# Kernel tuning notes

Measured on AMD Instinct MI355X. Metric: run time of the kernel, lower is better.

The kernel has to match this reference:

```python
import jax, jax.numpy as jnp
import numpy as np

NUM_HEADS = 8
WINDOW = 3
LOCAL_LEN = WINDOW * WINDOW
SR_RATIO = 8


def _normalize(v, eps=1e-12):
    n = jnp.linalg.norm(v, axis=-1, keepdims=True)
    return v / jnp.maximum(n, eps)


def _layernorm(v, g, b, eps=1e-5):
    m = v.mean(-1, keepdims=True)
    var = ((v - m) ** 2).mean(-1, keepdims=True)
    return (v - m) / jnp.sqrt(var + eps) * g + b


def _unfold3(x, H, W):
    # x: [B, C, H, W] -> [B, C, 9, H*W]  (kernel 3, pad 1, stride 1; torch nn.Unfold layout)
    B, C = x.shape[0], x.shape[1]
    xp = jnp.pad(x, ((0, 0), (0, 0), (1, 1), (1, 1)))
    patches = jnp.stack([xp[:, :, di:di + H, dj:dj + W]
                         for di in range(WINDOW) for dj in range(WINDOW)], axis=2)
    return patches.reshape(B, C, LOCAL_LEN, H * W)


def _forward(x, relative_coords_table, seq_length_scale, q_w, q_b, kv_w, kv_b,
             temperature, query_embedding, sr_w, sr_b, norm_g, norm_b,
             cpb_fc1_w, cpb_fc1_b, cpb_fc2_w, cpb_fc2_b,
             rel_bias_local, learnable_tokens, learnable_bias,
             proj_w, proj_b, relative_pos_index, padding_mask, H, W):
    B, N, C = x.shape
    hd = C // NUM_HEADS
    pool_H, pool_W = H // SR_RATIO, W // SR_RATIO
    pool_len = pool_H * pool_W

    # ---- queries ----
    q = (x @ q_w.T + q_b).reshape(B, N, NUM_HEADS, hd).transpose(0, 2, 1, 3)  # [B,h,N,d]
    q_norm = _normalize(q)
    q_scaled = (q_norm + query_embedding) * jax.nn.softplus(temperature) * seq_length_scale

    # ---- local k/v via unfold ----
    kv = x @ kv_w.T + kv_b  # [B,N,2C]
    k_loc = _normalize(kv[..., :C].reshape(B, N, NUM_HEADS, hd)).reshape(B, N, C)
    kv_img = jnp.concatenate([k_loc, kv[..., C:]], -1).transpose(0, 2, 1).reshape(B, 2 * C, H, W)
    kv_unf = _unfold3(kv_img, H, W).reshape(B, 2 * NUM_HEADS, hd, LOCAL_LEN, N)
    kv_unf = kv_unf.transpose(0, 1, 4, 2, 3)  # [B,2h,N,d,9]
    k_local, v_local = kv_unf[:, :NUM_HEADS], kv_unf[:, NUM_HEADS:]

    attn_local = jnp.einsum('bhnd,bhndl->bhnl', q_scaled, k_local) + rel_bias_local[:, None, :]
    attn_local = jnp.where(padding_mask, -jnp.inf, attn_local)

    # ---- pooled global k/v ----
    x_img = x.transpose(0, 2, 1).reshape(B, C, H, W)
    x_sr = jax.nn.gelu(jnp.einsum('oc,bchw->bohw', sr_w, x_img) + sr_b[None, :, None, None],
                       approximate=False)
    x_pool = x_sr.reshape(B, C, pool_H, SR_RATIO, pool_W, SR_RATIO).mean((3, 5))
    x_pool = x_pool.reshape(B, C, pool_len).transpose(0, 2, 1)
    x_pool = _layernorm(x_pool, norm_g, norm_b)
    kv_p = (x_pool @ kv_w.T + kv_b).reshape(B, pool_len, 2 * NUM_HEADS, hd).transpose(0, 2, 1, 3)
    k_pool, v_pool = kv_p[:, :NUM_HEADS], kv_p[:, NUM_HEADS:]

    # ---- continuous relative position bias (extrapolation path) ----
    cpb = jax.nn.relu(relative_coords_table @ cpb_fc1_w.T + cpb_fc1_b) @ cpb_fc2_w.T + cpb_fc2_b  # [T,h]
    pool_bias = cpb[relative_pos_index].reshape(N, pool_len, NUM_HEADS).transpose(2, 0, 1)  # [h,N,P]

    attn_pool = jnp.einsum('bhnd,bhpd->bhnp', q_scaled, _normalize(k_pool)) + pool_bias

    attn = jax.nn.softmax(jnp.concatenate([attn_local, attn_pool], -1), axis=-1)
    a_loc, a_pool = attn[..., :LOCAL_LEN], attn[..., LOCAL_LEN:]

    lt = jnp.einsum('bhnd,hdl->bhnl', q_norm, learnable_tokens) + learnable_bias + a_loc
    x_local = jnp.einsum('bhnl,bhndl->bhnd', lt, v_local)
    x_p = jnp.einsum('bhnp,bhpd->bhnd', a_pool, v_pool)
    out = (x_local + x_p).transpose(0, 2, 1, 3).reshape(B, N, C)
    return out @ proj_w.T + proj_b


def setup_inputs() -> dict:
    key = jax.random.key(0)
    B, H, W, C = 4, 64, 64, 256
    N = H * W
    hd = C // NUM_HEADS
    pool_H, pool_W = H // SR_RATIO, W // SR_RATIO
    pool_len = pool_H * pool_W

    # padding mask + per-query valid window length (get_seqlen_and_mask)
    ii, jj = np.meshgrid(np.arange(H), np.arange(W), indexing='ij')
    cols = []
    for di in range(WINDOW):
        for dj in range(WINDOW):
            ni, nj = ii + di - 1, jj + dj - 1
            cols.append(((ni < 0) | (ni >= H) | (nj < 0) | (nj >= W)).reshape(-1))
    padding_mask = np.stack(cols, -1)  # [N, 9], True = outside image
    local_len = (~padding_mask).sum(-1, keepdims=True).astype(np.float32)
    seq_length_scale = np.log(local_len + pool_len)  # [N, 1]

    # get_relative_position_cpb((H,W), (pool_H,pool_W))
    axis_q = np.arange(H, dtype=np.float64)
    axis_k = axis_q.reshape(pool_H, SR_RATIO).mean(-1)
    kh, kw = np.meshgrid(axis_k, axis_k, indexing='ij')
    qh, qw = np.meshgrid(axis_q, axis_q, indexing='ij')
    rel_h = (qh.ravel()[:, None] - kh.ravel()[None, :]) / (H - 1) * 8
    rel_w = (qw.ravel()[:, None] - kw.ravel()[None, :]) / (W - 1) * 8
    rel = np.stack([rel_h, rel_w], -1).reshape(-1, 2)
    table, idx = np.unique(rel, axis=0, return_inverse=True)
    table = np.sign(table) * np.log2(np.abs(table) + 1.0) / np.log2(8.0)

    ks = jax.random.split(key, 12)

    def nrm(k, shape, std=0.02):
        return jax.random.normal(k, shape, jnp.float32) * std

    return {
        'x': jax.random.normal(ks[0], (B, N, C), jnp.float32),
        'relative_coords_table': jnp.asarray(table, jnp.float32),
        'seq_length_scale': jnp.asarray(seq_length_scale, jnp.float32),
        'q_w': nrm(ks[1], (C, C)), 'q_b': jnp.zeros((C,), jnp.float32),
        'kv_w': nrm(ks[2], (2 * C, C)), 'kv_b': jnp.zeros((2 * C,), jnp.float32),
        'temperature': jnp.full((NUM_HEADS, 1, 1), float(np.log(np.expm1(1.0 / 0.24))), jnp.float32),
        'query_embedding': nrm(ks[3], (NUM_HEADS, 1, hd)),
        'sr_w': nrm(ks[4], (C, C)), 'sr_b': jnp.zeros((C,), jnp.float32),
        'norm_g': jnp.ones((C,), jnp.float32), 'norm_b': jnp.zeros((C,), jnp.float32),
        'cpb_fc1_w': nrm(ks[5], (512, 2), 0.1), 'cpb_fc1_b': jnp.zeros((512,), jnp.float32),
        'cpb_fc2_w': nrm(ks[6], (NUM_HEADS, 512)), 'cpb_fc2_b': jnp.zeros((NUM_HEADS,), jnp.float32),
        'rel_bias_local': nrm(ks[7], (NUM_HEADS, LOCAL_LEN), 0.0004),
        'learnable_tokens': nrm(ks[8], (NUM_HEADS, hd, LOCAL_LEN)),
        'learnable_bias': jnp.zeros((NUM_HEADS, 1, LOCAL_LEN), jnp.float32),
        'proj_w': nrm(ks[9], (C, C)), 'proj_b': jnp.zeros((C,), jnp.float32),
        'relative_pos_index': jnp.asarray(idx, jnp.int32),
        'padding_mask': jnp.asarray(padding_mask),
        'H': H, 'W': W,
    }


def reference(x, relative_coords_table, seq_length_scale, q_w, q_b, kv_w, kv_b,
              temperature, query_embedding, sr_w, sr_b, norm_g, norm_b,
              cpb_fc1_w, cpb_fc1_b, cpb_fc2_w, cpb_fc2_b,
              rel_bias_local, learnable_tokens, learnable_bias,
              proj_w, proj_b, relative_pos_index, padding_mask, H, W):
    return _forward(x, relative_coords_table, seq_length_scale, q_w, q_b, kv_w, kv_b,
                    temperature, query_embedding, sr_w, sr_b, norm_g, norm_b,
                    cpb_fc1_w, cpb_fc1_b, cpb_fc2_w, cpb_fc2_b,
                    rel_bias_local, learnable_tokens, learnable_bias,
                    proj_w, proj_b, relative_pos_index, padding_mask, H, W)
```

## Files before the change

### kernel.cpp

```cpp
#include <hip/hip_runtime.h>
#include <math.h>


typedef unsigned short ushort_t;
typedef __attribute__((ext_vector_type(8))) _Float16 half8;
typedef __attribute__((ext_vector_type(2))) _Float16 half2_t;
typedef __attribute__((ext_vector_type(4))) float f32x4;

static __device__ __forceinline__ ushort_t f2h(float f) {
    _Float16 h = (_Float16)f;
    return *(ushort_t*)&h;
}

static __device__ __forceinline__ float fdot2f(half2_t a, half2_t b, float c) {
#if __has_builtin(__builtin_amdgcn_fdot2)
    return __builtin_amdgcn_fdot2(a, b, c, false);
#else
    return (float)a[0] * (float)b[0] + (float)a[1] * (float)b[1] + c;
#endif
}

template <int CTRL>
static __device__ __forceinline__ float dpp_addf(float x) {
    int v = __builtin_amdgcn_update_dpp(
        0, __builtin_bit_cast(int, x), CTRL, 0xF, 0xF, true);
    return x + __builtin_bit_cast(float, v);
}
static __device__ __forceinline__ float quad_sumf(float x) {
    return dpp_addf<0x4E>(dpp_addf<0xB1>(x));
}
static __device__ __forceinline__ float sum16f(float x) {
    return dpp_addf<0x128>(dpp_addf<0x124>(quad_sumf(x)));
}

#define GLOAD16(g, l)                                                        \
    __builtin_amdgcn_global_load_lds(                                        \
        (const __attribute__((address_space(1))) unsigned int*)(g),          \
        (__attribute__((address_space(3))) unsigned int*)(l), 16, 0, 0)

template <int TM, int TN, bool AHM>
__global__ __launch_bounds__(256) void mfma_hgemm(
    const ushort_t* __restrict__ Ag, const ushort_t* __restrict__ Bg,
    const float* __restrict__ bias, float* __restrict__ out0,
    ushort_t* __restrict__ qh_out, ushort_t* __restrict__ kvh,
    ushort_t* __restrict__ xsrh, int mode, int Arows)
{
    const int K = 256;
    const int IM = TM / 32;
    const int JN = TN / 32;
    constexpr int LPS = TM / 64 + TN / 64;
    __shared__ ushort_t Ah[2][TM * 32];
    __shared__ ushort_t Bh[2][TN * 32];

    const int t = threadIdx.x;
    const int w = t >> 6;
    const int lane = t & 63;

    const int nwg = gridDim.x * gridDim.y;
    int wg = blockIdx.y * gridDim.x + blockIdx.x;
    wg = (wg & 7) * (nwg >> 3) + (wg >> 3);
    const int bm = (wg / gridDim.x) * TM;
    const int bn = (wg % gridDim.x) * TN;

    const int wm = (w >> 1) * (TM / 2);
    const int wn = (w & 1) * (TN / 2);

    f32x4 acc[IM][JN];
#pragma unroll
    for (int i = 0; i < IM; ++i)
#pragma unroll
        for (int j = 0; j < JN; ++j) acc[i][j] = f32x4{0.f, 0.f, 0.f, 0.f};

    const int lrow  = t >> 2;
    const int lk8sw = ((t & 3) ^ ((t >> 3) & 3)) * 8;

#define STAGE(bufi, k0s)                                                     \
    do {                                                                     \
        _Pragma("unroll")                                                    \
        for (int r = 0; r < TM / 64; ++r) {                                  \
            const ushort_t* srcA = AHM                                       \
                ? Ag + ((size_t)((k0s) >> 5) * Arows + (bm + r * 64 + lrow)) * 32 + lk8sw \
                : Ag + (size_t)(bm + r * 64 + lrow) * K + (k0s) + lk8sw;     \
            GLOAD16(srcA, &Ah[bufi][(unsigned)(r * 64 + w * 16) * 32]);      \
        }                                                                    \
        _Pragma("unroll")                                                    \
        for (int r = 0; r < TN / 64; ++r)                                    \
            GLOAD16(Bg + (size_t)(bn + r * 64 + lrow) * K + (k0s) + lk8sw,   \
                    &Bh[bufi][(unsigned)(r * 64 + w * 16) * 32]);            \
    } while (0)

    const int fr   = lane & 15;
    const int sws8 = ((lane >> 4) ^ ((fr >> 1) & 3)) * 8;

#define COMPUTE(bufi)                                                        \
    do {                                                                     \
        half8 af[IM], bf[JN];                                                \
        _Pragma("unroll")                                                    \
        for (int i2 = 0; i2 < IM; ++i2)                                      \
            af[i2] = *(const half8*)&Ah[bufi][(unsigned)(wm + i2 * 16 + fr) * 32 + sws8]; \
        _Pragma("unroll")                                                    \
        for (int j2 = 0; j2 < JN; ++j2)                                      \
            bf[j2] = *(const half8*)&Bh[bufi][(unsigned)(wn + j2 * 16 + fr) * 32 + sws8]; \
        __builtin_amdgcn_s_setprio(1);                                       \
        _Pragma("unroll")                                                    \
        for (int i2 = 0; i2 < IM; ++i2)                                      \
            _Pragma("unroll")                                                \
            for (int j2 = 0; j2 < JN; ++j2)                                  \
                acc[i2][j2] = __builtin_amdgcn_mfma_f32_16x16x32_f16(        \
                    af[i2], bf[j2], acc[i2][j2], 0, 0, 0);                   \
        __builtin_amdgcn_s_setprio(0);                                       \
    } while (0)

    STAGE(0, 0);
    STAGE(1, 32);
    int buf = 0;
#pragma unroll
    for (int s = 0; s < K / 32 - 1; ++s) {
        asm volatile("s_waitcnt vmcnt(%0)" :: "n"(LPS) : "memory");
        __builtin_amdgcn_s_barrier();
        asm volatile("" ::: "memory");
        COMPUTE(buf);
        asm volatile("" ::: "memory");
        __builtin_amdgcn_s_barrier();
        asm volatile("" ::: "memory");
        if (s + 2 < K / 32) STAGE(buf, (s + 2) * 32);
        buf ^= 1;
    }
    asm volatile("s_waitcnt vmcnt(0)" ::: "memory");
    __builtin_amdgcn_s_barrier();
    asm volatile("" ::: "memory");
    COMPUTE(buf);
#undef COMPUTE
#undef STAGE

    const int q4 = (lane >> 4) * 4;
#pragma unroll
    for (int i = 0; i < IM; ++i) {
#pragma unroll
        for (int jp = 0; jp < JN / 2; ++jp) {
#pragma unroll
            for (int r = 0; r < 4; ++r) {
                const int row = bm + wm + i * 16 + q4 + r;
                const int col0 = bn + wn + jp * 32 + fr;
                const int col1 = col0 + 16;
                float v0 = acc[i][2 * jp][r] + bias[col0];
                float v1 = acc[i][2 * jp + 1][r] + bias[col1];
                if (mode == 0) {
                    if (col0 < 256) {
                        const size_t base = ((size_t)(col0 >> 5) * Arows + row) * 32;
                        qh_out[base + fr]      = f2h(v0);
                        qh_out[base + fr + 16] = f2h(v1);
                    } else if (col0 < 512) {
                        const float ss = sum16f(v0 * v0 + v1 * v1);
                        const float invn = 1.0f / fmaxf(sqrtf(ss), 1e-12f);
                        const size_t base = ((size_t)((col0 - 256) >> 5) * Arows + row) * 64;
                        kvh[base + fr]      = f2h(v0 * invn);
                        kvh[base + fr + 16] = f2h(v1 * invn);
                    } else if (col0 < 768) {
                        const size_t base = ((size_t)((col0 - 512) >> 5) * Arows + row) * 64 + 32;
                        kvh[base + fr]      = f2h(v0);
                        kvh[base + fr + 16] = f2h(v1);
                    } else {
                        v0 = 0.5f * v0 * (1.0f + erff(v0 * 0.70710678118654752f));
                        v1 = 0.5f * v1 * (1.0f + erff(v1 * 0.70710678118654752f));
                        xsrh[(size_t)row * 256 + (col0 - 768)] = f2h(v0);
                        xsrh[(size_t)row * 256 + (col1 - 768)] = f2h(v1);
                    }
                } else if (mode == 2) {
                    if (col0 < 256) {
                        const float ss = sum16f(v0 * v0 + v1 * v1);
                        const float invn = 1.0f / fmaxf(sqrtf(ss), 1e-12f);
                        const size_t base = ((size_t)(col0 >> 5) * Arows + row) * 64;
                        kvh[base + fr]      = f2h(v0 * invn);
                        kvh[base + fr + 16] = f2h(v1 * invn);
                    } else {
                        const size_t base = ((size_t)((col0 - 256) >> 5) * Arows + row) * 64 + 32;
                        kvh[base + fr]      = f2h(v0);
                        kvh[base + fr + 16] = f2h(v1);
                    }
                } else {
                    out0[(size_t)row * 256 + col0] = v0;
                    out0[(size_t)row * 256 + col1] = v1;
                }
            }
        }
    }
}

__global__ __launch_bounds__(256) void prep_cpb(
    const float4* __restrict__ x, ushort4* __restrict__ xh, int n4, int nprep,
    const float* __restrict__ qw, const float* __restrict__ kvw,
    const float* __restrict__ srw, const float* __restrict__ pw,
    const float* __restrict__ qb, const float* __restrict__ kvb,
    const float* __restrict__ srb,
    ushort_t* __restrict__ Wall, ushort_t* __restrict__ Pw,
    float* __restrict__ ball,
    const float* __restrict__ table, const float* __restrict__ w1,
    const float* __restrict__ b1, const float* __restrict__ w2,
    const float* __restrict__ b2, float* __restrict__ outc, int T)
{
    if (blockIdx.x >= nprep) {
        const int wv = threadIdx.x >> 6;
        const int lane = threadIdx.x & 63;
        const int row = (blockIdx.x - nprep) * 4 + wv;
        if (row >= T) return;
        const float t0 = table[(size_t)row * 2];
        const float t1 = table[(size_t)row * 2 + 1];
        const int base = lane * 8;

        const float4* w1p = (const float4*)(w1 + (size_t)base * 2);
        float4 wa = w1p[0], wb = w1p[1], wc = w1p[2], wd = w1p[3];
        float4 ba = *(const float4*)(b1 + base);
        float4 bb = *(const float4*)(b1 + base + 4);
        float h[8];
        h[0] = fmaxf(fmaf(t1, wa.y, fmaf(t0, wa.x, ba.x)), 0.f);
        h[1] = fmaxf(fmaf(t1, wa.w, fmaf(t0, wa.z, ba.y)), 0.f);
        h[2] = fmaxf(fmaf(t1, wb.y, fmaf(t0, wb.x, ba.z)), 0.f);
        h[3] = fmaxf(fmaf(t1, wb.w, fmaf(t0, wb.z, ba.w)), 0.f);
        h[4] = fmaxf(fmaf(t1, wc.y, fmaf(t0, wc.x, bb.x)), 0.f);
        h[5] = fmaxf(fmaf(t1, wc.w, fmaf(t0, wc.z, bb.y)), 0.f);
        h[6] = fmaxf(fmaf(t1, wd.y, fmaf(t0, wd.x, bb.z)), 0.f);
        h[7] = fmaxf(fmaf(t1, wd.w, fmaf(t0, wd.z, bb.w)), 0.f);

#pragma unroll
        for (int hh = 0; hh < 8; ++hh) {
            const float4* w2p = (const float4*)(w2 + (size_t)hh * 512 + base);
            float4 p0 = w2p[0], p1 = w2p[1];
            float s = h[0]*p0.x + h[1]*p0.y + h[2]*p0.z + h[3]*p0.w
                    + h[4]*p1.x + h[5]*p1.y + h[6]*p1.z + h[7]*p1.w;
#pragma unroll
            for (int off = 1; off <= 32; off <<= 1) s += __shfl_xor(s, off);
            if (lane == 0) outc[(size_t)row * 8 + hh] = s + b2[hh];
        }
        return;
    }

    int idx = blockIdx.x * 256 + threadIdx.x;
    if (idx < n4) {
        float4 v = x[idx];
        ushort4 h;
        h.x = f2h(v.x); h.y = f2h(v.y); h.z = f2h(v.z); h.w = f2h(v.w);
        xh[idx] = h;
    }
    if (idx < 262144) {
        int nn = idx >> 8, k = idx & 255;
        float a;
        if (nn < 256)      a = qw[nn * 256 + k];
        else if (nn < 768) a = kvw[(nn - 256) * 256 + k];
        else               a = srw[(nn - 768) * 256 + k];
        Wall[idx] = f2h(a);
    }
    if (idx < 65536) Pw[idx] = f2h(pw[idx]);
    if (idx < 1024) {
        float bv;
        if (idx < 256)      bv = qb[idx];
        else if (idx < 768) bv = kvb[idx - 256];
        else                bv = srb[idx - 768];
        ball[idx] = bv;
    }
}

__global__ __launch_bounds__(256) void pool_ln(
    const ushort_t* __restrict__ xsr, const float* __restrict__ g,
    const float* __restrict__ be, ushort_t* __restrict__ xpool, int Hh, int Ww)
{
    const int C = 256;
    const int Nn = Hh * Ww;
    int b = blockIdx.x >> 6;
    int pidx = blockIdx.x & 63;
    int ph = pidx >> 3, pw = pidx & 7;
    int tid = threadIdx.x;
    float s = 0.f;
    for (int si = 0; si < 8; ++si) {
        int i = ph * 8 + si;
        const ushort_t* rowp = xsr + ((size_t)b * Nn + (size_t)i * Ww + pw * 8) * C + tid;
#pragma unroll
        for (int sj = 0; sj < 8; ++sj)
            s += (float)(*(const _Float16*)&rowp[(size_t)sj * C]);
    }
    s *= (1.f / 64.f);
    __shared__ float red[256];
    red[tid] = s; __syncthreads();
    for (int st = 128; st; st >>= 1) { if (tid < st) red[tid] += red[tid + st]; __syncthreads(); }
    float mean = red[0] * (1.f / 256.f);
    __syncthreads();
    float dv = s - mean;
    red[tid] = dv * dv; __syncthreads();
    for (int st = 128; st; st >>= 1) { if (tid < st) red[tid] += red[tid + st]; __syncthreads(); }
    float var = red[0] * (1.f / 256.f);
    xpool[(size_t)blockIdx.x * C + tid] = f2h(dv * rsqrtf(var + 1e-5f) * g[tid] + be[tid]);
}

__global__ __launch_bounds__(256) void attn_v9(
    const ushort_t* __restrict__ qh_g,
    const ushort_t* __restrict__ kvh,
    const ushort_t* __restrict__ kvph,
    const int* __restrict__ rpi,
    const float* __restrict__ cpbB,
    const float* __restrict__ sls, const float* __restrict__ temp,
    const float* __restrict__ qe, const float* __restrict__ rbl,
    const float* __restrict__ ltok, const float* __restrict__ lbias,
    ushort_t* __restrict__ attno,
    int Mtot)
{
    const int h = blockIdx.y, b = blockIdx.z;
    const int t = threadIdx.x;
    const int i = blockIdx.x;
    const int w = t >> 6;
    const int lane = t & 63;

    __shared__ ushort_t kvloc[3 * 64 * 64];
    __shared__ ushort_t kvp[64 * 64];
    __shared__ ushort_t pb_s[64][66];
    __shared__ float lts[9][32];
    __shared__ float rbl_s[9], lb_s[9], qe_s[32];

    {
        const int lt8 = lane >> 3, ls = lane & 7;
#pragma unroll
        for (int it = 0; it < 6; ++it) {
            const int u = it * 4 + w;
            const int dr = u >> 3, kB = u & 7;
            const int srcRow = min(max(i - 1 + dr, 0), 63);
            const int tok = kB * 8 + lt8;
            GLOAD16(kvh + ((size_t)h * Mtot + b * 4096 + srcRow * 64) * 64
                        + (size_t)(tok * 8 + (ls ^ (tok & 7))) * 8,
                    &kvloc[(size_t)(dr * 64 + kB * 8) * 64]);
        }
#pragma unroll
        for (int it = 0; it < 2; ++it) {
            const int u = it * 4 + w;
            const int tok = u * 8 + lt8;
            GLOAD16(kvph + ((size_t)h * 256 + b * 64) * 64
                         + (size_t)(tok * 8 + (ls ^ (tok & 7))) * 8,
                    &kvp[(size_t)(u * 8) * 64]);
        }
    }
    {
        const int rbase = i * 4096;
        for (int u = t; u < 4096; u += 256) {
            const int idx = rpi[rbase + u];
            pb_s[u >> 6][u & 63] = f2h(cpbB[(size_t)idx * 8 + h]);
        }
        for (int u = t; u < 288; u += 256) lts[u % 9][u / 9] = ltok[h * 288 + u];
        if (t < 9)  { rbl_s[t] = rbl[h * 9 + t]; lb_s[t] = lbias[h * 9 + t]; }
        if (t >= 64 && t < 96) qe_s[t - 64] = qe[h * 32 + (t - 64)];
    }
    __syncthreads();

    const int qi = lane >> 2;
    const int g4 = lane & 3;
    const int co = g4 * 8;
    const int j = w * 16 + qi;
    const int n = i * 64 + j;
    const size_t gq = (size_t)b * 4096 + n;

    const float tm = temp[h];
    const float sp = (tm > 20.f) ? tm : log1pf(expf(tm));

    float qv[8];
    {
        const half8 q8 = *(const half8*)(qh_g + ((size_t)h * Mtot + gq) * 32 + co);
        float ss = 0.f;
#pragma unroll
        for (int d = 0; d < 8; ++d) { qv[d] = (float)q8[d]; ss += qv[d] * qv[d]; }
        ss = quad_sumf(ss);
        const float invn = 1.0f / fmaxf(sqrtf(ss), 1e-12f);
#pragma unroll
        for (int d = 0; d < 8; ++d) qv[d] *= invn;
    }

    float lt[9];
#pragma unroll
    for (int l = 0; l < 9; ++l) {
        float dl = 0.f;
        const float4* lw = (const float4*)&lts[l][co];
#pragma unroll
        for (int c4 = 0; c4 < 2; ++c4) {
            float4 w4 = lw[c4];
            dl += qv[4*c4+0]*w4.x + qv[4*c4+1]*w4.y + qv[4*c4+2]*w4.z + qv[4*c4+3]*w4.w;
        }
        dl = quad_sumf(dl);
        lt[l] = dl + lb_s[l];
    }

    const float scal = sp * sls[n];
    half2_t qh[4];
#pragma unroll
    for (int c = 0; c < 4; ++c) {
        float a = (qv[2*c+0] + qe_s[co + 2*c+0]) * scal;
        float bq = (qv[2*c+1] + qe_s[co + 2*c+1]) * scal;
        qh[c] = half2_t{(_Float16)a, (_Float16)bq};
    }

    float sl[9];
#pragma unroll
    for (int l = 0; l < 9; ++l) {
        const int di = l / 3 - 1, dj = l % 3 - 1;
        const int ii = i + di;
        const int jn = j + dj;
        const bool ok = (ii >= 0) && (ii < 64) && (jn >= 0) && (jn < 64);
        const int dr = di + 1;
        const int tokc = max(min(jn, 63), 0);
        const half8 k8 = *(const half8*)
            &kvloc[(size_t)((dr * 64 + tokc) * 8 + (g4 ^ (tokc & 7))) * 8];
        float dk = 0.f;
        dk = fdot2f(qh[0], __builtin_shufflevector(k8, k8, 0, 1), dk);
        dk = fdot2f(qh[1], __builtin_shufflevector(k8, k8, 2, 3), dk);
        dk = fdot2f(qh[2], __builtin_shufflevector(k8, k8, 4, 5), dk);
        dk = fdot2f(qh[3], __builtin_shufflevector(k8, k8, 6, 7), dk);
        dk = quad_sumf(dk);
        sl[l] = ok ? (dk + rbl_s[l]) : -INFINITY;
    }

    float m = sl[0];
#pragma unroll
    for (int l = 1; l < 9; ++l) m = fmaxf(m, sl[l]);

    half2_t oh[4];
#pragma unroll
    for (int c = 0; c < 4; ++c) oh[c] = half2_t{(_Float16)0.f, (_Float16)0.f};
    float Z = 0.f;

    for (int cch = 0; cch < 8; ++cch) {
        float s8[8];
        float pbv[8];
#pragma unroll
        for (int c = 0; c < 4; ++c) {
            const half2_t p2 = *(const half2_t*)&pb_s[j][cch * 8 + 2 * c];
            pbv[2*c]   = (float)p2[0];
            pbv[2*c+1] = (float)p2[1];
        }
#pragma unroll
        for (int k = 0; k < 8; ++k) {
            const int p = cch * 8 + k;
            const half8 k8 = *(const half8*)
                &kvp[(size_t)(p * 8 + (g4 ^ (p & 7))) * 8];
            float acc = 0.f;
            acc = fdot2f(qh[0], __builtin_shufflevector(k8, k8, 0, 1), acc);
            acc = fdot2f(qh[1], __builtin_shufflevector(k8, k8, 2, 3), acc);
            acc = fdot2f(qh[2], __builtin_shufflevector(k8, k8, 4, 5), acc);
            acc = fdot2f(qh[3], __builtin_shufflevector(k8, k8, 6, 7), acc);
            acc = quad_sumf(acc);
            s8[k] = acc + pbv[k];
        }
        float cmax = s8[0];
#pragma unroll
        for (int k = 1; k < 8; ++k) cmax = fmaxf(cmax, s8[k]);
        const float m_new = fmaxf(m, cmax);
        const float factor = __expf(m - m_new);
        Z *= factor;
        const _Float16 fh = (_Float16)factor;
        const half2_t f2 = half2_t{fh, fh};
#pragma unroll
        for (int c = 0; c < 4; ++c) oh[c] *= f2;
        m = m_new;
#pragma unroll
        for (int k = 0; k < 8; ++k) {
            const float a = __expf(s8[k] - m);
            Z += a;
            const int p = cch * 8 + k;
            const _Float16 ah = (_Float16)a;
            const half2_t a2 = half2_t{ah, ah};
            const half8 v8 = *(const half8*)
                &kvp[(size_t)(p * 8 + ((4 + g4) ^ (p & 7))) * 8];
            oh[0] = a2 * __builtin_shufflevector(v8, v8, 0, 1) + oh[0];
            oh[1] = a2 * __builtin_shufflevector(v8, v8, 2, 3) + oh[1];
            oh[2] = a2 * __builtin_shufflevector(v8, v8, 4, 5) + oh[2];
            oh[3] = a2 * __builtin_shufflevector(v8, v8, 6, 7) + oh[3];
        }
    }

#pragma unroll
    for (int l = 0; l < 9; ++l) { sl[l] = __expf(sl[l] - m); Z += sl[l]; }

#pragma unroll
    for (int l = 0; l < 9; ++l) {
        const int di = l / 3 - 1, dj = l % 3 - 1;
        const int ii = i + di;
        const int jn = j + dj;
        const bool ok = (ii >= 0) && (ii < 64) && (jn >= 0) && (jn < 64);
        const int dr = di + 1;
        const int tokc = max(min(jn, 63), 0);
        const float coef = ok ? (sl[l] + lt[l] * Z) : 0.f;
        const half8 v8 = *(const half8*)
            &kvloc[(size_t)((dr * 64 + tokc) * 8 + ((4 + g4) ^ (tokc & 7))) * 8];
        const _Float16 ch = (_Float16)coef;
        const half2_t c2 = half2_t{ch, ch};
        oh[0] = c2 * __builtin_shufflevector(v8, v8, 0, 1) + oh[0];
        oh[1] = c2 * __builtin_shufflevector(v8, v8, 2, 3) + oh[1];
        oh[2] = c2 * __builtin_shufflevector(v8, v8, 4, 5) + oh[2];
        oh[3] = c2 * __builtin_shufflevector(v8, v8, 6, 7) + oh[3];
    }

    const float invZ = 1.0f / Z;
    ushort4* outp = (ushort4*)(attno + ((size_t)h * Mtot + gq) * 32 + co);
#pragma unroll
    for (int c4 = 0; c4 < 2; ++c4) {
        ushort4 u;
        u.x = f2h((float)oh[2*c4+0][0] * invZ);
        u.y = f2h((float)oh[2*c4+0][1] * invZ);
        u.z = f2h((float)oh[2*c4+1][0] * invZ);
        u.w = f2h((float)oh[2*c4+1][1] * invZ);
        outp[c4] = u;
    }
}

extern "C" void kernel_launch(void* const* d_in, const int* in_sizes, int n_in,
                              void* d_out, int out_size, void* d_ws, size_t ws_size,
                              hipStream_t stream)
{
    const float* x    = (const float*)d_in[0];
    const float* tbl  = (const float*)d_in[1];
    const float* sls  = (const float*)d_in[2];
    const float* q_w  = (const float*)d_in[3];
    const float* q_b  = (const float*)d_in[4];
    const float* kv_w = (const float*)d_in[5];
    const float* kv_b = (const float*)d_in[6];
    const float* temp = (const float*)d_in[7];
    const float* qe   = (const float*)d_in[8];
    const float* sr_w = (const float*)d_in[9];
    const float* sr_b = (const float*)d_in[10];
    const float* ng   = (const float*)d_in[11];
    const float* nb   = (const float*)d_in[12];
    const float* f1w  = (const float*)d_in[13];
    const float* f1b  = (const float*)d_in[14];
    const float* f2w  = (const float*)d_in[15];
    const float* f2b  = (const float*)d_in[16];
    const float* rbl  = (const float*)d_in[17];
    const float* ltok = (const float*)d_in[18];
    const float* lbias= (const float*)d_in[19];
    const float* pw   = (const float*)d_in[20];
    const float* pb   = (const float*)d_in[21];
    const int*   rpi  = (const int*)d_in[22];

    const int C = 256, Hh = 64, Ww = 64, Nn = Hh * Ww;
    const int B = in_sizes[0] / (Nn * C);
    const int T = in_sizes[1] / 2;
    const int M = B * Nn;

    float* ws = (float*)d_ws;
    size_t o = 0;
    ushort_t* qh    = (ushort_t*)(ws + o); o += (size_t)M * C / 2;
    ushort_t* kvh   = (ushort_t*)(ws + o); o += (size_t)M * C;
    ushort_t* xsrh  = (ushort_t*)(ws + o); o += (size_t)M * C / 2;
    ushort_t* xpoolh= (ushort_t*)(ws + o); o += (size_t)B * 64 * C / 2;
    ushort_t* kvph  = (ushort_t*)(ws + o); o += (size_t)B * 64 * C;
    float* cpbB  = ws + o; o += (size_t)T * 8;
    ushort_t* xh   = (ushort_t*)(ws + o); o += (size_t)M * C / 2;
    ushort_t* Wall = (ushort_t*)(ws + o); o += 1024 * 256 / 2;
    ushort_t* Pwh  = (ushort_t*)(ws + o); o += 256 * 256 / 2;
    float* ball = ws + o; o += 1024;
    ushort_t* attno_hf = xh;

    dim3 blk(256);
    const int n4x = M * C / 4;
    const int nprep = (n4x + 255) / 256;
    const int ncpb  = (T + 3) / 4;

    prep_cpb<<<nprep + ncpb, blk, 0, stream>>>(
        (const float4*)x, (ushort4*)xh, n4x,
        nprep, q_w, kv_w, sr_w, pw, q_b, kv_b, sr_b, Wall, Pwh, ball,
        tbl, f1w, f1b, f2w, f2b, cpbB, T);
    mfma_hgemm<128, 64, false><<<dim3(16, M / 128), blk, 0, stream>>>(
        xh, Wall, ball, nullptr, qh, kvh, xsrh, 0, M);
    pool_ln<<<B * 64, blk, 0, stream>>>(xsrh, ng, nb, xpoolh, Hh, Ww);
    mfma_hgemm<64, 64, false><<<dim3(8, (B * 64) / 64), blk, 0, stream>>>(
        xpoolh, Wall + 256 * 256, ball + 256, nullptr, nullptr, kvph, nullptr, 2, B * 64);
    attn_v9<<<dim3(64, 8, B), blk, 0, stream>>>(
        qh, kvh, kvph, rpi, cpbB, sls, temp, qe, rbl, ltok, lbias, attno_hf, M);
    mfma_hgemm<64, 64, true><<<dim3(4, M / 64), blk, 0, stream>>>(
        attno_hf, Pwh, pb, (float*)d_out, nullptr, nullptr, nullptr, 1, M);
}
```

Before: 219.3 us.

## Compute pooled attention scores with MFMA and precompute softmax probabilities in LDS

The per-thread fdot2 loop over 64 pooled keys, with its online softmax, is replaced by a per-wave 16x16x32 f16 MFMA that computes the query-by-pooled-key score tile, seeded with the position bias. Row max and sum come from DPP reductions, and the unnormalised probabilities go to a new LDS buffer along with per-row max and sum. The PV loop then only rescales the stored probabilities and accumulates V, which is meant to remove the scalar dot products and the repeated rescaling. It costs extra LDS, bpermute shuffles to build the MFMA A operand, and relies on the thread-to-row mapping matching across the MFMA layout and the later Ps[j] reads.

```diff
diff --git a/kernel.cpp b/kernel.cpp
--- a/kernel.cpp
+++ b/kernel.cpp
@@ -6,6 +6,7 @@
 typedef __attribute__((ext_vector_type(8))) _Float16 half8;
 typedef __attribute__((ext_vector_type(2))) _Float16 half2_t;
 typedef __attribute__((ext_vector_type(4))) float f32x4;
+typedef __attribute__((ext_vector_type(4))) int int4_t;
 
 static __device__ __forceinline__ ushort_t f2h(float f) {
     _Float16 h = (_Float16)f;
@@ -26,11 +27,20 @@
         0, __builtin_bit_cast(int, x), CTRL, 0xF, 0xF, true);
     return x + __builtin_bit_cast(float, v);
 }
+template <int CTRL>
+static __device__ __forceinline__ float dpp_maxf(float x) {
+    int v = __builtin_amdgcn_update_dpp(
+        0, __builtin_bit_cast(int, x), CTRL, 0xF, 0xF, true);
+    return fmaxf(x, __builtin_bit_cast(float, v));
+}
 static __device__ __forceinline__ float quad_sumf(float x) {
     return dpp_addf<0x4E>(dpp_addf<0xB1>(x));
 }
 static __device__ __forceinline__ float sum16f(float x) {
     return dpp_addf<0x128>(dpp_addf<0x124>(quad_sumf(x)));
+}
+static __device__ __forceinline__ float max16f(float x) {
+    return dpp_maxf<0x128>(dpp_maxf<0x124>(dpp_maxf<0x4E>(dpp_maxf<0xB1>(x))));
 }
 
 #define GLOAD16(g, l)                                                        \
@@ -291,7 +301,7 @@
     xpool[(size_t)blockIdx.x * C + tid] = f2h(dv * rsqrtf(var + 1e-5f) * g[tid] + be[tid]);
 }
 
-__global__ __launch_bounds__(256) void attn_v9(
+__global__ __launch_bounds__(256) void attn_v10(
     const ushort_t* __restrict__ qh_g,
     const ushort_t* __restrict__ kvh,
     const ushort_t* __restrict__ kvph,
@@ -312,6 +322,8 @@
     __shared__ ushort_t kvloc[3 * 64 * 64];
     __shared__ ushort_t kvp[64 * 64];
     __shared__ ushort_t pb_s[64][66];
+    __shared__ ushort_t Ps[64][72];
+    __shared__ float mzp[64][2];
     __shared__ float lts[9][32];
     __shared__ float rbl_s[9], lb_s[9], qe_s[32];
 
@@ -385,12 +397,12 @@
     }
 
     const float scal = sp * sls[n];
-    half2_t qh[4];
+    half2_t qhp[4];
 #pragma unroll
     for (int c = 0; c < 4; ++c) {
         float a = (qv[2*c+0] + qe_s[co + 2*c+0]) * scal;
         float bq = (qv[2*c+1] + qe_s[co + 2*c+1]) * scal;
-        qh[c] = half2_t{(_Float16)a, (_Float16)bq};
+        qhp[c] = half2_t{(_Float16)a, (_Float16)bq};
     }
 
     float sl[9];
@@ -405,62 +417,80 @@
         const half8 k8 = *(const half8*)
             &kvloc[(size_t)((dr * 64 + tokc) * 8 + (g4 ^ (tokc & 7))) * 8];
         float dk = 0.f;
-        dk = fdot2f(qh[0], __builtin_shufflevector(k8, k8, 0, 1), dk);
-        dk = fdot2f(qh[1], __builtin_shufflevector(k8, k8, 2, 3), dk);
-        dk = fdot2f(qh[2], __builtin_shufflevector(k8, k8, 4, 5), dk);
-        dk = fdot2f(qh[3], __builtin_shufflevector(k8, k8, 6, 7), dk);
+        dk = fdot2f(qhp[0], __builtin_shufflevector(k8, k8, 0, 1), dk);
+        dk = fdot2f(qhp[1], __builtin_shufflevector(k8, k8, 2, 3), dk);
+        dk = fdot2f(qhp[2], __builtin_shufflevector(k8, k8, 4, 5), dk);
+        dk = fdot2f(qhp[3], __builtin_shufflevector(k8, k8, 6, 7), dk);
         dk = quad_sumf(dk);
         sl[l] = ok ? (dk + rbl_s[l]) : -INFINITY;
     }
-
-    float m = sl[0];
-#pragma unroll
-    for (int l = 1; l < 9; ++l) m = fmaxf(m, sl[l]);
+    float m_l = sl[0];
+#pragma unroll
+    for (int l = 1; l < 9; ++l) m_l = fmaxf(m_l, sl[l]);
+
+    const int fr = lane & 15;
+    const int cn = lane >> 4;
+    const int q4 = cn * 4;
+    half8 af;
+    {
+        const int sidx = (4 * fr + cn) << 2;
+        int4_t ai;
+        ai.x = __builtin_amdgcn_ds_bpermute(sidx, __builtin_bit_cast(int, qhp[0]));
+        ai.y = __builtin_amdgcn_ds_bpermute(sidx, __builtin_bit_cast(int, qhp[1]));
+        ai.z = __builtin_amdgcn_ds_bpermute(sidx, __builtin_bit_cast(int, qhp[2]));
+        ai.w = __builtin_amdgcn_ds_bpermute(sidx, __builtin_bit_cast(int, qhp[3]));
+        af = __builtin_bit_cast(half8, ai);
+    }
+    f32x4 acc[4];
+#pragma unroll
+    for (int ct = 0; ct < 4; ++ct) {
+#pragma unroll
+        for (int r = 0; r < 4; ++r)
+            acc[ct][r] = (float)(*(const _Float16*)&pb_s[w * 16 + q4 + r][ct * 16 + fr]);
+    }
+#pragma unroll
+    for (int ct = 0; ct < 4; ++ct) {
+        const int tok = ct * 16 + fr;
+        const half8 bf = *(const half8*)&kvp[(size_t)(tok * 8 + (cn ^ (tok & 7))) * 8];
+        acc[ct] = __builtin_amdgcn_mfma_f32_16x16x32_f16(af, bf, acc[ct], 0, 0, 0);
+    }
+
+#pragma unroll
+    for (int r = 0; r < 4; ++r) {
+        float mm = fmaxf(fmaxf(acc[0][r], acc[1][r]), fmaxf(acc[2][r], acc[3][r]));
+        mm = max16f(mm);
+        float z = 0.f;
+        float pv[4];
+#pragma unroll
+        for (int ct = 0; ct < 4; ++ct) {
+            pv[ct] = __expf(acc[ct][r] - mm);
+            z += pv[ct];
+        }
+        z = sum16f(z);
+#pragma unroll
+        for (int ct = 0; ct < 4; ++ct)
+            Ps[w * 16 + q4 + r][ct * 16 + fr] = f2h(pv[ct]);
+        if (fr == 0) { mzp[w * 16 + q4 + r][0] = mm; mzp[w * 16 + q4 + r][1] = z; }
+    }
+
+    const float m_p = mzp[j][0];
+    const float Z_p = mzp[j][1];
+    const float m = fmaxf(m_l, m_p);
+    const float fp = __expf(m_p - m);
+    float Z = Z_p * fp;
+    const _Float16 fh = (_Float16)fp;
 
     half2_t oh[4];
 #pragma unroll
     for (int c = 0; c < 4; ++c) oh[c] = half2_t{(_Float16)0.f, (_Float16)0.f};
-    float Z = 0.f;
-
+
+#pragma unroll
     for (int cch = 0; cch < 8; ++cch) {
-        float s8[8];
-        float pbv[8];
-#pragma unroll
-        for (int c = 0; c < 4; ++c) {
-            const half2_t p2 = *(const half2_t*)&pb_s[j][cch * 8 + 2 * c];
-            pbv[2*c]   = (float)p2[0];
-            pbv[2*c+1] = (float)p2[1];
-        }
+        const half8 p8 = *(const half8*)&Ps[j][cch * 8];
 #pragma unroll
         for (int k = 0; k < 8; ++k) {
             const int p = cch * 8 + k;
-            const half8 k8 = *(const half8*)
-                &kvp[(size_t)(p * 8 + (g4 ^ (p & 7))) * 8];
-            float acc = 0.f;
-            acc = fdot2f(qh[0], __builtin_shufflevector(k8, k8, 0, 1), acc);
-            acc = fdot2f(qh[1], __builtin_shufflevector(k8, k8, 2, 3), acc);
-            acc = fdot2f(qh[2], __builtin_shufflevector(k8, k8, 4, 5), acc);
-            acc = fdot2f(qh[3], __builtin_shufflevector(k8, k8, 6, 7), acc);
-            acc = quad_sumf(acc);
-            s8[k] = acc + pbv[k];
-        }
-        float cmax = s8[0];
-#pragma unroll
-        for (int k = 1; k < 8; ++k) cmax = fmaxf(cmax, s8[k]);
-        const float m_new = fmaxf(m, cmax);
-        const float factor = __expf(m - m_new);
-        Z *= factor;
-        const _Float16 fh = (_Float16)factor;
-        const half2_t f2 = half2_t{fh, fh};
-#pragma unroll
-        for (int c = 0; c < 4; ++c) oh[c] *= f2;
-        m = m_new;
-#pragma unroll
-        for (int k = 0; k < 8; ++k) {
-            const float a = __expf(s8[k] - m);
-            Z += a;
-            const int p = cch * 8 + k;
-            const _Float16 ah = (_Float16)a;
+            const _Float16 ah = p8[k] * fh;
             const half2_t a2 = half2_t{ah, ah};
             const half8 v8 = *(const half8*)
                 &kvp[(size_t)(p * 8 + ((4 + g4) ^ (p & 7))) * 8];
@@ -567,7 +597,7 @@
     pool_ln<<<B * 64, blk, 0, stream>>>(xsrh, ng, nb, xpoolh, Hh, Ww);
     mfma_hgemm<64, 64, false><<<dim3(8, (B * 64) / 64), blk, 0, stream>>>(
         xpoolh, Wall + 256 * 256, ball + 256, nullptr, nullptr, kvph, nullptr, 2, B * 64);
-    attn_v9<<<dim3(64, 8, B), blk, 0, stream>>>(
+    attn_v10<<<dim3(64, 8, B), blk, 0, stream>>>(
         qh, kvh, kvph, rpi, cpbB, sls, temp, qe, rbl, ltok, lbias, attno_hf, M);
     mfma_hgemm<64, 64, true><<<dim3(4, M / 64), blk, 0, stream>>>(
         attno_hf, Pwh, pb, (float*)d_out, nullptr, nullptr, nullptr, 1, M);
```

After: 212.1 us. 3.2% less time.
